# Kernel optimization log

Hardware: AMD Instinct MI355X
Metric: run time of the kernel (lower is better)

## Reference

```python
import jax, jax.numpy as jnp
import numpy as np

N = 12288  # points in image 0
M = 12288  # points in image 1
D = 128    # descriptor dim
TEMP_SQRT_INV = 1.0 / np.sqrt(0.1)  # temperature = 0.1, applied to each descriptor


def setup_inputs() -> dict:
    key = jax.random.key(0)
    k0, k1, k2, k3, k4, k5 = jax.random.split(key, 6)
    desc_0 = jax.random.normal(k0, (N, D), jnp.float32)
    desc_0 = desc_0 / jnp.linalg.norm(desc_0, axis=-1, keepdims=True)
    desc_1 = jax.random.normal(k1, (M, D), jnp.float32)
    desc_1 = desc_1 / jnp.linalg.norm(desc_1, axis=-1, keepdims=True)
    # correspondence indices; -1 means "no correspondence"
    corr_0 = jax.random.randint(k2, (N,), -1, M, dtype=jnp.int64 if jax.config.jax_enable_x64 else jnp.int32)
    corr_1 = jax.random.randint(k3, (M,), -1, N, dtype=jnp.int64 if jax.config.jax_enable_x64 else jnp.int32)
    logits_0 = jax.random.normal(k4, (N,), jnp.float32)
    logits_1 = jax.random.normal(k5, (M,), jnp.float32)
    return {"desc_0": desc_0, "desc_1": desc_1, "corr_0": corr_0,
            "corr_1": corr_1, "logits_0": logits_0, "logits_1": logits_1}


def reference(desc_0, desc_1, corr_0, corr_1, logits_0, logits_1):
    # temperature scaling (module scales both descriptor sets by 1/sqrt(T))
    d0 = desc_0 * TEMP_SQRT_INV
    d1 = desc_1 * TEMP_SQRT_INV
    # dense similarity matrix [N, M] (the blockwise kernel target)
    S = jnp.einsum('nd,md->nm', d0, d1)

    m0 = corr_0 >= 0
    m1 = corr_1 >= 0
    i0 = jnp.clip(corr_0, 0)
    i1 = jnp.clip(corr_1, 0)

    # bidirectional InfoNCE cross-entropy (rows for image0, cols for image1)
    lse_0 = jax.nn.logsumexp(S, axis=1)               # [N]
    lse_1 = jax.nn.logsumexp(S, axis=0)               # [M]
    pos_0 = jnp.take_along_axis(S, i0[:, None], axis=1)[:, 0]  # S[i, corr_0[i]]
    pos_1 = S[i1, jnp.arange(M)]                                # S[corr_1[j], j]
    l0 = jnp.where(m0, lse_0 - pos_0, 0.0)
    l1 = jnp.where(m1, lse_1 - pos_1, 0.0)
    loss_0 = l0.sum() / jnp.maximum(m0.sum(), 1)
    loss_1 = l1.sum() / jnp.maximum(m1.sum(), 1)

    # mutual-nearest-neighbor matching + logit-gated precision/recall
    best_0 = jnp.argmax(S, axis=1)                    # [N] best match in image 1
    best_1 = jnp.argmax(S, axis=0)                    # [M] best match in image 0
    mutual = best_1[best_0] == jnp.arange(N)
    kp0 = jax.nn.sigmoid(logits_0) >= 0.5
    kp1 = jax.nn.sigmoid(logits_1) >= 0.5
    predicted = mutual & kp0 & kp1[best_0]
    correct = (best_0 == corr_0) & m0
    tp = (correct & predicted).sum()
    precision = tp / jnp.maximum(predicted.sum(), 1)
    recall = tp / jnp.maximum(m0.sum(), 1)
    return loss_0, loss_1, precision, recall
```

## Files before the change

kernel.cpp:

```cpp
#include <hip/hip_runtime.h>
#include <hip/hip_bf16.h>

#define NPTS 12288
#define DD 128
#define CHUNKS 8
#define CHW (NPTS / CHUNKS)
#define TILES (CHW / 64)
#define NBG (NPTS / 128)

#define PRESCALE 3.79828262f

typedef short bf16x8 __attribute__((ext_vector_type(8)));
typedef float f32x4 __attribute__((ext_vector_type(4)));

__device__ __forceinline__ float fast_exp2(float x) {
#if defined(__has_builtin)
#if __has_builtin(__builtin_amdgcn_exp2f)
  return __builtin_amdgcn_exp2f(x);
#else
  return exp2f(x);
#endif
#else
  return exp2f(x);
#endif
}

__device__ __forceinline__ short f2bf(float f) {
  unsigned u = __float_as_uint(f);
  u += 0x7FFFu + ((u >> 16) & 1u);
  return (short)(u >> 16);
}

__device__ __forceinline__ unsigned umax(unsigned a, unsigned b) { return a > b ? a : b; }

__global__ void k_conv(const float* __restrict__ d0, const float* __restrict__ d1,
                       short* __restrict__ o0, short* __restrict__ o1) {
  unsigned t = blockIdx.x * 256u + threadIdx.x;
  const unsigned half = (NPTS * DD) / 4;
  const float* src; short* dst; unsigned g;
  if (t < half) { src = d0; dst = o0; g = t; }
  else          { src = d1; dst = o1; g = t - half; }
  float4 v = *(const float4*)(src + (size_t)g * 4);
  short4 r;
  r.x = f2bf(v.x * PRESCALE); r.y = f2bf(v.y * PRESCALE);
  r.z = f2bf(v.z * PRESCALE); r.w = f2bf(v.w * PRESCALE);
  *(short4*)(dst + (size_t)g * 4) = r;
}

__launch_bounds__(256, 3)
__global__ void k_main(const short* __restrict__ d0b, const short* __restrict__ d1b,
                       uint2* __restrict__ colKV, uint2* __restrict__ rowKV) {
  __shared__ __align__(16) char bLds[2][16384];
  __shared__ uint2 crLds[2][4][64];
  const int widx = threadIdx.x >> 6;
  const int lane = threadIdx.x & 63;
  const int lo = lane & 15, hi = lane >> 4;
  const int chunk = blockIdx.x & (CHUNKS - 1);
  const int bg = blockIdx.x >> 3;
  const int row0 = bg * 128 + widx * 32;
  const int cbase = chunk * CHW;

  const char* btile0 = (const char*)(d1b + (size_t)cbase * DD);

  #define STAGE(tt, bb) do {                                                   \
    const char* gsrc_ = btile0 + (size_t)(tt) * 16384;                         \
    _Pragma("unroll")                                                          \
    for (int it_ = 0; it_ < 4; it_++) {                                        \
      int L_ = (widx << 12) + (it_ << 10) + (lane << 4);                       \
      int so_ = L_ ^ (((L_ >> 8) & 15) << 4);                                  \
      __builtin_amdgcn_global_load_lds((const void*)(gsrc_ + so_),             \
          (void*)(&bLds[bb][(widx << 12) + (it_ << 10)]), 16, 0, 0);           \
    }                                                                          \
  } while (0)

  bf16x8 af[2][4];
  #pragma unroll
  for (int i = 0; i < 2; i++)
    #pragma unroll
    for (int kk = 0; kk < 4; kk++)
      af[i][kk] = *(const bf16x8*)(d0b + (size_t)(row0 + i * 16 + lo) * DD + kk * 32 + hi * 8);

  float rowsum[2][4], rowkeyf[2][4];
  #pragma unroll
  for (int i = 0; i < 2; i++)
    #pragma unroll
    for (int r = 0; r < 4; r++) {
      rowsum[i][r] = 0.f;
      rowkeyf[i][r] = 0.f;
    }
  const unsigned rcbase = 0x3FFFu - (unsigned)(row0 + hi * 4);
  const int axor = lo << 4;

  STAGE(0, 0);
  __syncthreads();

  #pragma unroll 1
  for (int t = 0; t < TILES; t++) {
    const int cur = t & 1;
    if (t + 1 < TILES) STAGE(t + 1, cur ^ 1);

    f32x4 acc[2][4];
    #pragma unroll
    for (int i = 0; i < 2; i++)
      #pragma unroll
      for (int j = 0; j < 4; j++)
        acc[i][j] = (f32x4){0.f, 0.f, 0.f, 0.f};

    const char* bbuf = &bLds[cur][0];
    #pragma unroll
    for (int kk = 0; kk < 4; kk++) {
      bf16x8 bfr[4];
      #pragma unroll
      for (int j = 0; j < 4; j++) {
        int bbyte = (((j << 4) + lo) << 8) + (kk << 6) + (hi << 4);
        bbyte ^= axor;
        bfr[j] = *(const bf16x8*)(bbuf + bbyte);
      }
      #pragma unroll
      for (int j = 0; j < 4; j++)
        #pragma unroll
        for (int i = 0; i < 2; i++)
          acc[i][j] = __builtin_amdgcn_mfma_f32_16x16x32_bf16(af[i][kk], bfr[j], acc[i][j], 0, 0, 0);
    }

    const int ct = cbase + t * 64;
    #pragma unroll
    for (int j = 0; j < 4; j++) {
      float es[8], ck[8];
      const unsigned ccomp = 0x3FFFu - (unsigned)(ct + j * 16 + lo);
      #pragma unroll
      for (int i = 0; i < 2; i++)
        #pragma unroll
        for (int r = 0; r < 4; r++) {
          float e = fast_exp2(acc[i][j][r]);
          unsigned tb = __float_as_uint(e) & 0xFFFFC000u;
          rowkeyf[i][r] = fmaxf(rowkeyf[i][r], __uint_as_float(tb | ccomp));
          ck[i * 4 + r] = __uint_as_float(tb | (rcbase - (unsigned)(i * 16 + r)));
          es[i * 4 + r] = e;
          rowsum[i][r] += e;
        }
      float colsum = ((es[0] + es[1]) + (es[2] + es[3])) +
                     ((es[4] + es[5]) + (es[6] + es[7]));
      float colkeyf = fmaxf(fmaxf(fmaxf(ck[0], ck[1]), fmaxf(ck[2], ck[3])),
                            fmaxf(fmaxf(ck[4], ck[5]), fmaxf(ck[6], ck[7])));
      colsum += __shfl_xor(colsum, 16, 64);
      colsum += __shfl_xor(colsum, 32, 64);
      colkeyf = fmaxf(colkeyf, __shfl_xor(colkeyf, 16, 64));
      colkeyf = fmaxf(colkeyf, __shfl_xor(colkeyf, 32, 64));
      if (hi == 0)
        crLds[cur][widx][j * 16 + lo] = make_uint2(__float_as_uint(colkeyf), __float_as_uint(colsum));
    }

    __syncthreads();

    if (lane < 16) {
      int c = widx * 16 + lane;
      uint2 p0 = crLds[cur][0][c], p1 = crLds[cur][1][c];
      uint2 p2 = crLds[cur][2][c], p3 = crLds[cur][3][c];
      float s = (__uint_as_float(p0.y) + __uint_as_float(p1.y)) +
                (__uint_as_float(p2.y) + __uint_as_float(p3.y));
      float k = fmaxf(fmaxf(__uint_as_float(p0.x), __uint_as_float(p1.x)),
                      fmaxf(__uint_as_float(p2.x), __uint_as_float(p3.x)));
      colKV[(size_t)bg * NPTS + ct + c] = make_uint2(__float_as_uint(k), __float_as_uint(s));
    }
  }

  #pragma unroll
  for (int i = 0; i < 2; i++)
    #pragma unroll
    for (int r = 0; r < 4; r++) {
      float s = rowsum[i][r];
      float k = rowkeyf[i][r];
      s += __shfl_xor(s, 1, 64); s += __shfl_xor(s, 2, 64);
      s += __shfl_xor(s, 4, 64); s += __shfl_xor(s, 8, 64);
      k = fmaxf(k, __shfl_xor(k, 1, 64));
      k = fmaxf(k, __shfl_xor(k, 2, 64));
      k = fmaxf(k, __shfl_xor(k, 4, 64));
      k = fmaxf(k, __shfl_xor(k, 8, 64));
      if (lo == 0) {
        int row = row0 + i * 16 + hi * 4 + r;
        rowKV[(size_t)chunk * NPTS + row] = make_uint2(__float_as_uint(k), __float_as_uint(s));
      }
    }
  #undef STAGE
}

__global__ void k_red(const uint2* __restrict__ colKV, const uint2* __restrict__ rowKV,
                      const float* __restrict__ d0, const float* __restrict__ d1,
                      const int* __restrict__ c0, const int* __restrict__ c1,
                      unsigned* __restrict__ best0, unsigned* __restrict__ best1,
                      float* __restrict__ l0part, float* __restrict__ l1part) {
  float v;
  if (blockIdx.x < 48) {
    int m = blockIdx.x * 256 + threadIdx.x;
    float s = 0.f; unsigned k = 0u;
    #pragma unroll 8
    for (int b = 0; b < NBG; b++) {
      uint2 kv = colKV[(size_t)b * NPTS + m];
      s += __uint_as_float(kv.y);
      k = umax(k, kv.x);
    }
    best1[m] = 0x3FFFu - (k & 0x3FFFu);
    int cc = c1[m];
    int i = cc > 0 ? cc : 0;
    const float4* pa = (const float4*)(d0 + (size_t)i * DD);
    const float4* pb = (const float4*)(d1 + (size_t)m * DD);
    float dot = 0.f;
    #pragma unroll 8
    for (int q = 0; q < DD / 4; q++) {
      float4 a = pa[q], b = pb[q];
      dot += a.x * b.x + a.y * b.y + a.z * b.z + a.w * b.w;
    }
    v = (cc >= 0) ? (logf(s) - 10.0f * dot) : 0.f;
  } else {
    int n = (blockIdx.x - 48) * 256 + threadIdx.x;
    float s = 0.f; unsigned k = 0u;
    #pragma unroll
    for (int c = 0; c < CHUNKS; c++) {
      uint2 kv = rowKV[(size_t)c * NPTS + n];
      s += __uint_as_float(kv.y);
      k = umax(k, kv.x);
    }
    best0[n] = 0x3FFFu - (k & 0x3FFFu);
    int cc = c0[n];
    int i = cc > 0 ? cc : 0;
    const float4* pa = (const float4*)(d0 + (size_t)n * DD);
    const float4* pb = (const float4*)(d1 + (size_t)i * DD);
    float dot = 0.f;
    #pragma unroll 8
    for (int q = 0; q < DD / 4; q++) {
      float4 a = pa[q], b = pb[q];
      dot += a.x * b.x + a.y * b.y + a.z * b.z + a.w * b.w;
    }
    v = (cc >= 0) ? (logf(s) - 10.0f * dot) : 0.f;
  }
  __shared__ float red[256];
  red[threadIdx.x] = v; __syncthreads();
  for (int st = 128; st > 0; st >>= 1) {
    if (threadIdx.x < st) red[threadIdx.x] += red[threadIdx.x + st];
    __syncthreads();
  }
  if (threadIdx.x == 0) {
    if (blockIdx.x < 48) l1part[blockIdx.x] = red[0];
    else                 l0part[blockIdx.x - 48] = red[0];
  }
}

__global__ void k_stats(const int* __restrict__ c0, const int* __restrict__ c1,
                        const float* __restrict__ lg0, const float* __restrict__ lg1,
                        const unsigned* __restrict__ best0, const unsigned* __restrict__ best1,
                        int4* __restrict__ statpart) {
  int n = blockIdx.x * 256 + threadIdx.x;
  int cc = c0[n];
  bool m0 = cc >= 0;
  int b0 = (int)best0[n];
  bool mutual = ((int)best1[b0] == n);
  bool pred = mutual && (lg0[n] >= 0.f) && (lg1[b0] >= 0.f);
  int4 v;
  v.x = m0 ? 1 : 0;
  v.y = (c1[n] >= 0) ? 1 : 0;
  v.z = (pred && m0 && b0 == cc) ? 1 : 0;
  v.w = pred ? 1 : 0;
  __shared__ int4 red[256];
  red[threadIdx.x] = v; __syncthreads();
  for (int st = 128; st > 0; st >>= 1) {
    if (threadIdx.x < st) {
      int4 o = red[threadIdx.x + st];
      red[threadIdx.x].x += o.x; red[threadIdx.x].y += o.y;
      red[threadIdx.x].z += o.z; red[threadIdx.x].w += o.w;
    }
    __syncthreads();
  }
  if (threadIdx.x == 0) statpart[blockIdx.x] = red[0];
}

__global__ void k_final(const float* __restrict__ l0part, const float* __restrict__ l1part,
                        const int4* __restrict__ statpart, float* __restrict__ out) {
  const int tid = threadIdx.x;
  float l0s = 0.f, l1s = 0.f;
  int4 st = make_int4(0, 0, 0, 0);
  if (tid < 48) {
    l0s = l0part[tid]; l1s = l1part[tid];
    st = statpart[tid];
  }
  #pragma unroll
  for (int off = 32; off >= 1; off >>= 1) {
    l0s += __shfl_down(l0s, off, 64);
    l1s += __shfl_down(l1s, off, 64);
    st.x += __shfl_down(st.x, off, 64);
    st.y += __shfl_down(st.y, off, 64);
    st.z += __shfl_down(st.z, off, 64);
    st.w += __shfl_down(st.w, off, 64);
  }
  if (tid == 0) {
    int M0 = st.x > 0 ? st.x : 1;
    int M1 = st.y > 0 ? st.y : 1;
    int PR = st.w > 0 ? st.w : 1;
    out[0] = l0s / (float)M0;
    out[1] = l1s / (float)M1;
    out[2] = (float)st.z / (float)PR;
    out[3] = (float)st.z / (float)M0;
  }
}

extern "C" void kernel_launch(void* const* d_in, const int* in_sizes, int n_in,
                              void* d_out, int out_size, void* d_ws, size_t ws_size,
                              hipStream_t stream) {
  const float* desc0 = (const float*)d_in[0];
  const float* desc1 = (const float*)d_in[1];
  const int* corr0   = (const int*)d_in[2];
  const int* corr1   = (const int*)d_in[3];
  const float* lg0   = (const float*)d_in[4];
  const float* lg1   = (const float*)d_in[5];
  float* out = (float*)d_out;

  char* w = (char*)d_ws;
  short* d0b   = (short*)(w);
  short* d1b   = (short*)(w + 3145728);
  uint2* colKV = (uint2*)(w + 6291456);
  uint2* rowKV = (uint2*)(w + 15728640);
  unsigned* best0 = (unsigned*)(w + 16515072);
  unsigned* best1 = (unsigned*)(w + 16564224);
  float* l0part = (float*)(w + 16613376);
  float* l1part = (float*)(w + 16613568);
  int4* statpart = (int4*)(w + 16613760);

  k_conv<<<3072, 256, 0, stream>>>(desc0, desc1, d0b, d1b);
  k_main<<<768, 256, 0, stream>>>(d0b, d1b, colKV, rowKV);
  k_red<<<96, 256, 0, stream>>>(colKV, rowKV, desc0, desc1, corr0, corr1, best0, best1, l0part, l1part);
  k_stats<<<48, 256, 0, stream>>>(corr0, corr1, lg0, lg1, best0, best1, statpart);
  k_final<<<1, 64, 0, stream>>>(l0part, l1part, statpart, out);
}
```

Before: 111.6 us.

## Drop LDS staging and block barriers; write per-wave column partials directly

Removes the shared-memory double buffer for desc_1 tiles and has each wave load B fragments straight from global memory (relying on L1/L2 reuse across the four waves). The per-tile __syncthreads and cross-wave column reduction are removed too. Each wave now writes its own 32-row band partials to colKV, which grows fourfold and shifts the workspace layout. The reduction kernel now loops over 384 bands instead of 96. This trades barrier stalls for more global and cache traffic and a heavier column reduction.

```diff
diff --git a/kernel.cpp b/kernel.cpp
--- a/kernel.cpp
+++ b/kernel.cpp
@@ -6,7 +6,7 @@
 #define CHUNKS 8
 #define CHW (NPTS / CHUNKS)
 #define TILES (CHW / 64)
-#define NBG (NPTS / 128)
+#define NBANDS (NPTS / 32)
 
 #define PRESCALE 3.79828262f
 
@@ -50,28 +50,13 @@
 __launch_bounds__(256, 3)
 __global__ void k_main(const short* __restrict__ d0b, const short* __restrict__ d1b,
                        uint2* __restrict__ colKV, uint2* __restrict__ rowKV) {
-  __shared__ __align__(16) char bLds[2][16384];
-  __shared__ uint2 crLds[2][4][64];
   const int widx = threadIdx.x >> 6;
   const int lane = threadIdx.x & 63;
   const int lo = lane & 15, hi = lane >> 4;
   const int chunk = blockIdx.x & (CHUNKS - 1);
-  const int bg = blockIdx.x >> 3;
-  const int row0 = bg * 128 + widx * 32;
+  const int band = (blockIdx.x >> 3) * 4 + widx;
+  const int row0 = band * 32;
   const int cbase = chunk * CHW;
-
-  const char* btile0 = (const char*)(d1b + (size_t)cbase * DD);
-
-  #define STAGE(tt, bb) do {                                                   \
-    const char* gsrc_ = btile0 + (size_t)(tt) * 16384;                         \
-    _Pragma("unroll")                                                          \
-    for (int it_ = 0; it_ < 4; it_++) {                                        \
-      int L_ = (widx << 12) + (it_ << 10) + (lane << 4);                       \
-      int so_ = L_ ^ (((L_ >> 8) & 15) << 4);                                  \
-      __builtin_amdgcn_global_load_lds((const void*)(gsrc_ + so_),             \
-          (void*)(&bLds[bb][(widx << 12) + (it_ << 10)]), 16, 0, 0);           \
-    }                                                                          \
-  } while (0)
 
   bf16x8 af[2][4];
   #pragma unroll
@@ -89,15 +74,12 @@
       rowkeyf[i][r] = 0.f;
     }
   const unsigned rcbase = 0x3FFFu - (unsigned)(row0 + hi * 4);
-  const int axor = lo << 4;
-
-  STAGE(0, 0);
-  __syncthreads();
+
+  const short* bp0 = d1b + (size_t)cbase * DD;
 
   #pragma unroll 1
   for (int t = 0; t < TILES; t++) {
-    const int cur = t & 1;
-    if (t + 1 < TILES) STAGE(t + 1, cur ^ 1);
+    const short* bpt = bp0 + (size_t)t * 64 * DD;
 
     f32x4 acc[2][4];
     #pragma unroll
@@ -106,16 +88,12 @@
       for (int j = 0; j < 4; j++)
         acc[i][j] = (f32x4){0.f, 0.f, 0.f, 0.f};
 
-    const char* bbuf = &bLds[cur][0];
     #pragma unroll
     for (int kk = 0; kk < 4; kk++) {
       bf16x8 bfr[4];
       #pragma unroll
-      for (int j = 0; j < 4; j++) {
-        int bbyte = (((j << 4) + lo) << 8) + (kk << 6) + (hi << 4);
-        bbyte ^= axor;
-        bfr[j] = *(const bf16x8*)(bbuf + bbyte);
-      }
+      for (int j = 0; j < 4; j++)
+        bfr[j] = *(const bf16x8*)(bpt + (size_t)(j * 16 + lo) * DD + kk * 32 + hi * 8);
       #pragma unroll
       for (int j = 0; j < 4; j++)
         #pragma unroll
@@ -148,20 +126,8 @@
       colkeyf = fmaxf(colkeyf, __shfl_xor(colkeyf, 16, 64));
       colkeyf = fmaxf(colkeyf, __shfl_xor(colkeyf, 32, 64));
       if (hi == 0)
-        crLds[cur][widx][j * 16 + lo] = make_uint2(__float_as_uint(colkeyf), __float_as_uint(colsum));
-    }
-
-    __syncthreads();
-
-    if (lane < 16) {
-      int c = widx * 16 + lane;
-      uint2 p0 = crLds[cur][0][c], p1 = crLds[cur][1][c];
-      uint2 p2 = crLds[cur][2][c], p3 = crLds[cur][3][c];
-      float s = (__uint_as_float(p0.y) + __uint_as_float(p1.y)) +
-                (__uint_as_float(p2.y) + __uint_as_float(p3.y));
-      float k = fmaxf(fmaxf(__uint_as_float(p0.x), __uint_as_float(p1.x)),
-                      fmaxf(__uint_as_float(p2.x), __uint_as_float(p3.x)));
-      colKV[(size_t)bg * NPTS + ct + c] = make_uint2(__float_as_uint(k), __float_as_uint(s));
+        colKV[(size_t)band * NPTS + ct + j * 16 + lo] =
+            make_uint2(__float_as_uint(colkeyf), __float_as_uint(colsum));
     }
   }
 
@@ -182,7 +148,6 @@
         rowKV[(size_t)chunk * NPTS + row] = make_uint2(__float_as_uint(k), __float_as_uint(s));
       }
     }
-  #undef STAGE
 }
 
 __global__ void k_red(const uint2* __restrict__ colKV, const uint2* __restrict__ rowKV,
@@ -195,7 +160,7 @@
     int m = blockIdx.x * 256 + threadIdx.x;
     float s = 0.f; unsigned k = 0u;
     #pragma unroll 8
-    for (int b = 0; b < NBG; b++) {
+    for (int b = 0; b < NBANDS; b++) {
       uint2 kv = colKV[(size_t)b * NPTS + m];
       s += __uint_as_float(kv.y);
       k = umax(k, kv.x);
@@ -318,12 +283,12 @@
   short* d0b   = (short*)(w);
   short* d1b   = (short*)(w + 3145728);
   uint2* colKV = (uint2*)(w + 6291456);
-  uint2* rowKV = (uint2*)(w + 15728640);
-  unsigned* best0 = (unsigned*)(w + 16515072);
-  unsigned* best1 = (unsigned*)(w + 16564224);
-  float* l0part = (float*)(w + 16613376);
-  float* l1part = (float*)(w + 16613568);
-  int4* statpart = (int4*)(w + 16613760);
+  uint2* rowKV = (uint2*)(w + 44040192);
+  unsigned* best0 = (unsigned*)(w + 44826624);
+  unsigned* best1 = (unsigned*)(w + 44875776);
+  float* l0part = (float*)(w + 44924928);
+  float* l1part = (float*)(w + 44925120);
+  int4* statpart = (int4*)(w + 44925312);
 
   k_conv<<<3072, 256, 0, stream>>>(desc0, desc1, d0b, d1b);
   k_main<<<768, 256, 0, stream>>>(d0b, d1b, colKV, rowKV);
```

After: 182.2 us. 1.63x slower.
